# Optimization experiments

Hardware: AMD Instinct MI355X
Metric: run time of the kernel (lower is better)

Reference implementation:

```python
import jax, jax.numpy as jnp
import numpy as np

H, D = 8, 16
HD = H * D
SCALE0 = float(1.0 / np.sqrt(D * 1))   # degree-0 dot-product scale (order m=1)
SCALE1 = float(1.0 / np.sqrt(D * 3))   # degree-1 dot-product scale (order m=3)
SHARED = float(np.sqrt(0.5))           # shared_scale = sqrt(1/2) for DOT_PROD + SHARED
NEG = -1e9


def _split_heads_q(x):  # (b,n,HD,m) -> (b,H,n,D,m)
    b, n, _, m = x.shape
    return x.reshape(b, n, H, D, m).transpose(0, 2, 1, 3, 4)


def _split_heads_k(x):  # (b,n,N,HD,m) -> (b,H,n,N,D,m)
    b, n, N, _, m = x.shape
    return x.reshape(b, n, N, H, D, m).transpose(0, 3, 1, 2, 4, 5)


def _augment_kv(k, v, feats, W_self, null_k, null_v):
    # attend_self: VNLinear self key/value; use_null_kv: learned null tokens.
    b, n = feats.shape[:2]
    m = feats.shape[-1]
    skv = jnp.einsum('oc,bncm->bnom', W_self, feats)          # (b,n,2HD,m)
    sk, sv = jnp.split(skv, 2, axis=-2)
    sk = _split_heads_q(sk)[:, :, :, None]                     # (b,H,n,1,D,m)
    sv = _split_heads_q(sv)[:, :, :, None]
    nk = jnp.broadcast_to(null_k[None, :, None, None], (b, H, n, 1, D, m))
    nv = jnp.broadcast_to(null_v[None, :, None, None], (b, H, n, 1, D, m))
    k = jnp.concatenate([nk, sk, k], axis=3)                   # (b,H,n,2+N,D,m)
    v = jnp.concatenate([nv, sv, v], axis=3)
    return k, v


def _merge_heads(x):  # (b,H,n,D,m) -> (b,n,HD,m)
    b, _, n, _, m = x.shape
    return x.transpose(0, 2, 1, 3, 4).reshape(b, n, HD, m)


def _forward(q0, k0, v0, q1, k1, v1, feats0, feats1, edges,
             W_self_kv0, W_self_kv1, W_bias, self_bias, null_bias,
             null_k0, null_v0, null_k1, null_v1, head_weights1,
             W_out0, W_out1, neighbor_mask):
    b, n, N = edges.shape[:3]
    q0h, k0h, v0h = _split_heads_q(q0), _split_heads_k(k0), _split_heads_k(v0)
    q1h, k1h, v1h = _split_heads_q(q1), _split_heads_k(k1), _split_heads_k(v1)
    k0h, v0h = _augment_kv(k0h, v0h, feats0, W_self_kv0, null_k0, null_v0)
    k1h, v1h = _augment_kv(k1h, v1h, feats1, W_self_kv1, null_k1, null_v1)

    # pair bias for degree 0 (to_order==1); prepend null/self bias columns
    edge_bias = jnp.einsum('bnje,he->bhnj', edges, W_bias)     # (b,H,n,N)
    nb = jnp.broadcast_to(null_bias[None, :, None, None], (b, H, n, 1))
    sb = jnp.broadcast_to(self_bias[None, :, None, None], (b, H, n, 1))
    bias = jnp.concatenate([nb, sb, edge_bias], axis=-1)        # (b,H,n,2+N)

    sim0 = jnp.einsum('bhndm,bhnjdm->bhnj', q0h, k0h) * SCALE0 + bias
    w1 = jax.nn.softplus(head_weights1)                         # (1,H,1,1)
    sim1 = jnp.einsum('bhndm,bhnjdm->bhnj', q1h, k1h) * (SCALE1 * w1)

    total = (sim0 + sim1) * SHARED
    mask = jnp.concatenate(
        [jnp.ones((b, 1, n, 2), dtype=bool),                    # null + self always valid
         neighbor_mask[:, None]], axis=-1)
    total = jnp.where(mask, total, NEG)
    attn = jax.nn.softmax(total, axis=-1)                       # shared across degrees

    out0 = _merge_heads(jnp.einsum('bhnj,bhnjdm->bhndm', attn, v0h))
    out1 = _merge_heads(jnp.einsum('bhnj,bhnjdm->bhndm', attn, v1h))

    y0 = jnp.einsum('oc,bncm->bnom', W_out0, out0)              # FiberLinear deg 0
    y1 = jnp.einsum('oc,bncm->bnom', W_out1, out1)              # FiberLinear deg 1
    return y0, y1


def setup_inputs() -> dict:
    key = jax.random.key(0)
    ks = jax.random.split(key, 20)
    b, n, N, e = 1, 2048, 32, 32
    d0, d1 = 128, 64
    f = lambda k, s: jax.random.normal(k, s, dtype=jnp.float32) * 0.1
    return {
        'q0': f(ks[0], (b, n, HD, 1)), 'k0': f(ks[1], (b, n, N, HD, 1)), 'v0': f(ks[2], (b, n, N, HD, 1)),
        'q1': f(ks[3], (b, n, HD, 3)), 'k1': f(ks[4], (b, n, N, HD, 3)), 'v1': f(ks[5], (b, n, N, HD, 3)),
        'feats0': f(ks[6], (b, n, d0, 1)), 'feats1': f(ks[7], (b, n, d1, 3)),
        'edges': f(ks[8], (b, n, N, e)),
        'W_self_kv0': f(ks[9], (2 * HD, d0)), 'W_self_kv1': f(ks[10], (2 * HD, d1)),
        'W_bias': f(ks[11], (H, e)),
        'self_bias': jnp.zeros((H,), jnp.float32), 'null_bias': jnp.zeros((H,), jnp.float32),
        'null_k0': jnp.zeros((H, D, 1), jnp.float32), 'null_v0': jnp.zeros((H, D, 1), jnp.float32),
        'null_k1': jnp.zeros((H, D, 3), jnp.float32), 'null_v1': jnp.zeros((H, D, 3), jnp.float32),
        'head_weights1': jnp.full((1, H, 1, 1), float(np.log(np.e - 1.0)), jnp.float32),
        'W_out0': f(ks[12], (d0, HD)), 'W_out1': f(ks[13], (d1, HD)),
        'neighbor_mask': jax.random.uniform(ks[14], (b, n, N)) > 0.1,
    }


def reference(q0, k0, v0, q1, k1, v1, feats0, feats1, edges,
              W_self_kv0, W_self_kv1, W_bias, self_bias, null_bias,
              null_k0, null_v0, null_k1, null_v1, head_weights1,
              W_out0, W_out1, neighbor_mask):
    return _forward(q0, k0, v0, q1, k1, v1, feats0, feats1, edges,
                    W_self_kv0, W_self_kv1, W_bias, self_bias, null_bias,
                    null_k0, null_v0, null_k1, null_v1, head_weights1,
                    W_out0, W_out1, neighbor_mask)
```

## Files before the change

### kernel.cpp

```cpp
#include <hip/hip_runtime.h>
#include <hip/hip_bf16.h>

constexpr int kH  = 8;
constexpr int kD  = 16;
constexpr int kHD = 128;
constexpr int kN  = 32;
constexpr int kE  = 32;
constexpr int kD0 = 128;
constexpr int kD1 = 64;

constexpr float SCALE0   = 0.25f;
constexpr float SCALE1   = 0.14433756729740643f;
constexpr float SHARED_S = 0.70710678118654752f;
constexpr float NEGV     = -1e9f;

__global__ __launch_bounds__(256) void se3_attn_kernel(
    const float* __restrict__ q0, const float* __restrict__ k0, const float* __restrict__ v0,
    const float* __restrict__ q1, const float* __restrict__ k1, const float* __restrict__ v1,
    const float* __restrict__ feats0, const float* __restrict__ feats1,
    const float* __restrict__ edges,
    const float* __restrict__ Wskv0, const float* __restrict__ Wskv1,
    const float* __restrict__ Wbias, const float* __restrict__ self_bias,
    const float* __restrict__ null_bias,
    const float* __restrict__ nk0, const float* __restrict__ nv0,
    const float* __restrict__ nk1, const float* __restrict__ nv1,
    const float* __restrict__ hw1,
    const float* __restrict__ Wout0, const float* __restrict__ Wout1,
    const int* __restrict__ nmask,
    float* __restrict__ out, int n_total)
{
  const int i = blockIdx.x;
  const int t = threadIdx.x;

  __shared__ float q0s[kH * 17];
  __shared__ float q1s[kH * 49];
  __shared__ float f0s[kD0];
  __shared__ float f1s[kD1 * 3];
  __shared__ float edg[kN * 33];
  __shared__ float wbT[kE * kH];
  __shared__ float w1s[kH];
  __shared__ float sk0[kHD], sv0[kHD];
  __shared__ float sk1[kHD * 3], sv1[kHD * 3];
  __shared__ float sc[kH][34];
  __shared__ float o0[kHD];
  __shared__ float o1[kHD * 3];

  {
    if (t < kHD) {
      int h = t >> 4, d = t & 15;
      q0s[h * 17 + d] = q0[(size_t)i * kHD + t];
    }
    for (int u = t; u < kHD * 3; u += 256) {
      int c = u / 3, m = u - c * 3;
      int h = c >> 4, d = c & 15;
      q1s[h * 49 + d * 3 + m] = q1[(size_t)i * kHD * 3 + u];
    }
    if (t < kD0) f0s[t] = feats0[(size_t)i * kD0 + t];
    if (t < kD1 * 3) f1s[t] = feats1[(size_t)i * kD1 * 3 + t];
    for (int u = t; u < kN * kE; u += 256) {
      int j = u >> 5, e = u & 31;
      edg[j * 33 + e] = edges[(size_t)i * kN * kE + u];
    }
    if (t < kH * kE) {
      int h = t >> 5, e = t & 31;
      wbT[e * 8 + h] = Wbias[t];
    }
    if (t < kH) {
      float x = hw1[t];
      w1s[t] = log1pf(expf(x));
    }
  }
  __syncthreads();

  {
    const int o = t;
    float acc = 0.f;
    const float4* wrow = (const float4*)(Wskv0 + o * kD0);
    #pragma unroll
    for (int g = 0; g < 32; ++g) {
      float4 w = wrow[g];
      int cb = g * 4;
      acc += w.x * f0s[cb + 0] + w.y * f0s[cb + 1] + w.z * f0s[cb + 2] + w.w * f0s[cb + 3];
    }
    if (o < kHD) sk0[o] = acc; else sv0[o - kHD] = acc;
    float a0 = 0.f, a1 = 0.f, a2 = 0.f;
    const float4* wrow1 = (const float4*)(Wskv1 + o * kD1);
    #pragma unroll
    for (int g = 0; g < 16; ++g) {
      float4 w = wrow1[g];
      float wv[4] = {w.x, w.y, w.z, w.w};
      int cb = g * 4;
      #pragma unroll
      for (int q = 0; q < 4; ++q) {
        int c3 = (cb + q) * 3;
        a0 += wv[q] * f1s[c3 + 0];
        a1 += wv[q] * f1s[c3 + 1];
        a2 += wv[q] * f1s[c3 + 2];
      }
    }
    if (o < kHD) { sk1[o*3+0] = a0; sk1[o*3+1] = a1; sk1[o*3+2] = a2; }
    else { int p = (o - kHD) * 3; sv1[p+0] = a0; sv1[p+1] = a1; sv1[p+2] = a2; }
  }

  {
    const int j = t >> 3, h = t & 7;
    float bias = 0.f;
    #pragma unroll
    for (int e = 0; e < kE; ++e) bias += edg[j * 33 + e] * wbT[e * 8 + h];
    float s0 = 0.f;
    {
      const float4* kr = (const float4*)(k0 + (size_t)(i * kN + j) * kHD + h * kD);
      #pragma unroll
      for (int g = 0; g < 4; ++g) {
        float4 w = kr[g];
        int x = h * 17 + g * 4;
        s0 += w.x * q0s[x + 0] + w.y * q0s[x + 1] + w.z * q0s[x + 2] + w.w * q0s[x + 3];
      }
    }
    float s1 = 0.f;
    {
      const float4* kr1 = (const float4*)(k1 + (size_t)(i * kN + j) * kHD * 3 + h * 48);
      #pragma unroll
      for (int g = 0; g < 12; ++g) {
        float4 w = kr1[g];
        int x = h * 49 + g * 4;
        s1 += w.x * q1s[x + 0] + w.y * q1s[x + 1] + w.z * q1s[x + 2] + w.w * q1s[x + 3];
      }
    }
    float total = (s0 * SCALE0 + bias + s1 * SCALE1 * w1s[h]) * SHARED_S;
    bool valid = nmask[(size_t)i * kN + j] != 0;
    sc[h][2 + j] = valid ? total : NEGV;
  }
  __syncthreads();

  if (t < 2 * kH) {
    int h = t & 7;
    bool is_self = t >= kH;
    float s0 = 0.f, s1 = 0.f, bias;
    if (is_self) {
      #pragma unroll
      for (int d = 0; d < kD; ++d) s0 += q0s[h * 17 + d] * sk0[h * kD + d];
      #pragma unroll
      for (int x = 0; x < 48; ++x) s1 += q1s[h * 49 + x] * sk1[h * 48 + x];
      bias = self_bias[h];
    } else {
      #pragma unroll
      for (int d = 0; d < kD; ++d) s0 += q0s[h * 17 + d] * nk0[h * kD + d];
      #pragma unroll
      for (int x = 0; x < 48; ++x) s1 += q1s[h * 49 + x] * nk1[h * 48 + x];
      bias = null_bias[h];
    }
    float total = (s0 * SCALE0 + bias + s1 * SCALE1 * w1s[h]) * SHARED_S;
    sc[h][is_self ? 1 : 0] = total;
  }
  __syncthreads();

  if (t < kH) {
    float mx = -1e30f;
    #pragma unroll
    for (int j = 0; j < 34; ++j) mx = fmaxf(mx, sc[t][j]);
    float sum = 0.f;
    #pragma unroll
    for (int j = 0; j < 34; ++j) sum += __expf(sc[t][j] - mx);
    float inv = 1.f / sum;
    #pragma unroll
    for (int j = 0; j < 34; ++j) sc[t][j] = __expf(sc[t][j] - mx) * inv;
  }
  __syncthreads();

  if (t < 64) {
    const int c0 = 2 * t;
    const int h = t >> 3;
    float ax = sc[h][0] * nv0[c0]     + sc[h][1] * sv0[c0];
    float ay = sc[h][0] * nv0[c0 + 1] + sc[h][1] * sv0[c0 + 1];
    const float2* vp = (const float2*)(v0 + (size_t)i * kN * kHD) + t;
    #pragma unroll
    for (int j = 0; j < kN; ++j) {
      float2 p = vp[j * 64];
      float a = sc[h][2 + j];
      ax += a * p.x; ay += a * p.y;
    }
    o0[c0] = ax; o0[c0 + 1] = ay;
  } else {
    const int u = t - 64;
    const int f0i = 2 * u;
    const int h = u / 24;
    float ax = sc[h][0] * nv1[f0i]     + sc[h][1] * sv1[f0i];
    float ay = sc[h][0] * nv1[f0i + 1] + sc[h][1] * sv1[f0i + 1];
    const float2* vp = (const float2*)(v1 + (size_t)i * kN * kHD * 3) + u;
    #pragma unroll
    for (int j = 0; j < kN; ++j) {
      float2 p = vp[j * 192];
      float a = sc[h][2 + j];
      ax += a * p.x; ay += a * p.y;
    }
    o1[f0i] = ax; o1[f0i + 1] = ay;
  }
  __syncthreads();

  for (int u = t; u < 320; u += 256) {
    if (u < 128) {
      const int o = u;
      float acc = 0.f;
      const float4* wr = (const float4*)(Wout0 + o * kHD);
      #pragma unroll
      for (int g = 0; g < 32; ++g) {
        float4 w = wr[g];
        int cb = g * 4;
        acc += w.x * o0[cb + 0] + w.y * o0[cb + 1] + w.z * o0[cb + 2] + w.w * o0[cb + 3];
      }
      out[(size_t)i * kHD + o] = acc;
    } else {
      const int v2 = u - 128;
      const int o = v2 / 3, m = v2 - o * 3;
      float acc = 0.f;
      const float4* wr = (const float4*)(Wout1 + o * kHD);
      #pragma unroll
      for (int g = 0; g < 32; ++g) {
        float4 w = wr[g];
        int cb = g * 4;
        acc += w.x * o1[(cb + 0) * 3 + m] + w.y * o1[(cb + 1) * 3 + m]
             + w.z * o1[(cb + 2) * 3 + m] + w.w * o1[(cb + 3) * 3 + m];
      }
      out[(size_t)n_total * kHD + (size_t)i * 192 + v2] = acc;
    }
  }
}

extern "C" void kernel_launch(void* const* d_in, const int* in_sizes, int n_in,
                              void* d_out, int out_size, void* d_ws, size_t ws_size,
                              hipStream_t stream) {
  const int n = in_sizes[0] / kHD;
  se3_attn_kernel<<<n, 256, 0, stream>>>(
      (const float*)d_in[0],  (const float*)d_in[1],  (const float*)d_in[2],
      (const float*)d_in[3],  (const float*)d_in[4],  (const float*)d_in[5],
      (const float*)d_in[6],  (const float*)d_in[7],  (const float*)d_in[8],
      (const float*)d_in[9],  (const float*)d_in[10], (const float*)d_in[11],
      (const float*)d_in[12], (const float*)d_in[13], (const float*)d_in[14],
      (const float*)d_in[15], (const float*)d_in[16], (const float*)d_in[17],
      (const float*)d_in[18], (const float*)d_in[19], (const float*)d_in[20],
      (const int*)d_in[21],
      (float*)d_out, n);
}
```

Baseline: 379.2 us.

## Split fused attention kernel into three kernels staged through workspace

Splits the single per-node kernel into three launches: self key/value projection with null/self scores, neighbor similarity plus softmax, and value aggregation plus output projection. Intermediates (scores, self values) go through global workspace instead of shared memory. This may lower per-kernel register and shared-memory pressure and raise occupancy, at the cost of extra launches, global round trips, and reloading q in two kernels.

Result: slower. 389.6 us (+2.7%).

```diff
diff --git a/kernel.cpp b/kernel.cpp
--- a/kernel.cpp
+++ b/kernel.cpp
@@ -14,170 +14,197 @@
 constexpr float SHARED_S = 0.70710678118654752f;
 constexpr float NEGV     = -1e9f;
 
-__global__ __launch_bounds__(256) void se3_attn_kernel(
-    const float* __restrict__ q0, const float* __restrict__ k0, const float* __restrict__ v0,
-    const float* __restrict__ q1, const float* __restrict__ k1, const float* __restrict__ v1,
+
+__global__ __launch_bounds__(256) void k1_selfkv(
+    const float* __restrict__ q0, const float* __restrict__ q1,
     const float* __restrict__ feats0, const float* __restrict__ feats1,
-    const float* __restrict__ edges,
     const float* __restrict__ Wskv0, const float* __restrict__ Wskv1,
-    const float* __restrict__ Wbias, const float* __restrict__ self_bias,
-    const float* __restrict__ null_bias,
-    const float* __restrict__ nk0, const float* __restrict__ nv0,
-    const float* __restrict__ nk1, const float* __restrict__ nv1,
+    const float* __restrict__ self_bias, const float* __restrict__ null_bias,
+    const float* __restrict__ nk0, const float* __restrict__ nk1,
     const float* __restrict__ hw1,
+    float* __restrict__ ws_sc, float* __restrict__ ws_sv0, float* __restrict__ ws_sv1)
+{
+  const int i = blockIdx.x;
+  const int t = threadIdx.x;
+  __shared__ float f0s[kD0];
+  __shared__ float f1s[kD1 * 3];
+  __shared__ float q0s[kHD];
+  __shared__ float q1s[kHD * 3];
+  __shared__ float sk0[kHD];
+  __shared__ float sk1[kHD * 3];
+  __shared__ float w1s[kH];
+
+  if (t < kD0)     f0s[t] = feats0[(size_t)i * kD0 + t];
+  if (t < kD1 * 3) f1s[t] = feats1[(size_t)i * kD1 * 3 + t];
+  if (t < kHD)     q0s[t] = q0[(size_t)i * kHD + t];
+  for (int u = t; u < kHD * 3; u += 256) q1s[u] = q1[(size_t)i * kHD * 3 + u];
+  if (t < kH) w1s[t] = log1pf(expf(hw1[t]));
+  __syncthreads();
+
+  float acc = 0.f;
+  {
+    const float4* wr = (const float4*)(Wskv0 + t * kD0);
+    #pragma unroll
+    for (int g = 0; g < 32; ++g) {
+      float4 w = wr[g];
+      int c = g * 4;
+      acc += w.x * f0s[c] + w.y * f0s[c + 1] + w.z * f0s[c + 2] + w.w * f0s[c + 3];
+    }
+  }
+  float a0 = 0.f, a1 = 0.f, a2 = 0.f;
+  {
+    const float4* wr = (const float4*)(Wskv1 + t * kD1);
+    #pragma unroll
+    for (int g = 0; g < 16; ++g) {
+      float4 w = wr[g];
+      int c = g * 4;
+      a0 += w.x * f1s[(c + 0) * 3 + 0] + w.y * f1s[(c + 1) * 3 + 0]
+          + w.z * f1s[(c + 2) * 3 + 0] + w.w * f1s[(c + 3) * 3 + 0];
+      a1 += w.x * f1s[(c + 0) * 3 + 1] + w.y * f1s[(c + 1) * 3 + 1]
+          + w.z * f1s[(c + 2) * 3 + 1] + w.w * f1s[(c + 3) * 3 + 1];
+      a2 += w.x * f1s[(c + 0) * 3 + 2] + w.y * f1s[(c + 1) * 3 + 2]
+          + w.z * f1s[(c + 2) * 3 + 2] + w.w * f1s[(c + 3) * 3 + 2];
+    }
+  }
+  if (t < kHD) {
+    sk0[t] = acc;
+    sk1[t * 3 + 0] = a0; sk1[t * 3 + 1] = a1; sk1[t * 3 + 2] = a2;
+  } else {
+    const int o = t - kHD;
+    ws_sv0[(size_t)i * kHD + o] = acc;
+    float* sp = ws_sv1 + (size_t)i * kHD * 3 + o * 3;
+    sp[0] = a0; sp[1] = a1; sp[2] = a2;
+  }
+  __syncthreads();
+
+  if (t < 2 * kH) {
+    const int h = t & 7;
+    const bool is_self = t >= kH;
+    float s0 = 0.f, s1 = 0.f, bias;
+    if (is_self) {
+      #pragma unroll
+      for (int d = 0; d < kD; ++d) s0 += q0s[h * kD + d] * sk0[h * kD + d];
+      #pragma unroll
+      for (int x = 0; x < 48; ++x) s1 += q1s[h * 48 + x] * sk1[h * 48 + x];
+      bias = self_bias[h];
+    } else {
+      #pragma unroll
+      for (int d = 0; d < kD; ++d) s0 += q0s[h * kD + d] * nk0[h * kD + d];
+      #pragma unroll
+      for (int x = 0; x < 48; ++x) s1 += q1s[h * 48 + x] * nk1[h * 48 + x];
+      bias = null_bias[h];
+    }
+    float total = (s0 * SCALE0 + bias + s1 * SCALE1 * w1s[h]) * SHARED_S;
+    ws_sc[(size_t)i * 272 + h * 34 + (is_self ? 1 : 0)] = total;
+  }
+}
+
+__global__ __launch_bounds__(256) void k2_sims(
+    const float* __restrict__ q0, const float* __restrict__ q1,
+    const float* __restrict__ k0, const float* __restrict__ k1,
+    const float* __restrict__ edges, const float* __restrict__ Wbias,
+    const float* __restrict__ hw1, const int* __restrict__ nmask,
+    float* __restrict__ ws_sc)
+{
+  const int i = blockIdx.x;
+  const int t = threadIdx.x;
+  __shared__ float q0s[kH * 17];
+  __shared__ float q1s[kH * 49];
+  __shared__ float edg[kN * 33];
+  __shared__ float wbT[kE * kH];
+  __shared__ float w1s[kH];
+  __shared__ float scL[kH][34];
+
+  if (t < kHD) {
+    int h = t >> 4, d = t & 15;
+    q0s[h * 17 + d] = q0[(size_t)i * kHD + t];
+  }
+  for (int u = t; u < kHD * 3; u += 256) {
+    int c = u / 3, m = u - c * 3;
+    int h = c >> 4, d = c & 15;
+    q1s[h * 49 + d * 3 + m] = q1[(size_t)i * kHD * 3 + u];
+  }
+  for (int u = t; u < kN * kE; u += 256) {
+    int j = u >> 5, e = u & 31;
+    edg[j * 33 + e] = edges[(size_t)i * kN * kE + u];
+  }
+  if (t < kH * kE) {
+    int h = t >> 5, e = t & 31;
+    wbT[e * 8 + h] = Wbias[t];
+  }
+  if (t < kH) w1s[t] = log1pf(expf(hw1[t]));
+  if (t < 16) scL[t & 7][t >> 3] = ws_sc[(size_t)i * 272 + (t & 7) * 34 + (t >> 3)];
+  __syncthreads();
+
+  {
+    const int j = t >> 3, h = t & 7;
+    float bias = 0.f;
+    #pragma unroll
+    for (int e = 0; e < kE; ++e) bias += edg[j * 33 + e] * wbT[e * 8 + h];
+    float s0 = 0.f;
+    {
+      const float4* kr = (const float4*)(k0 + (size_t)(i * kN + j) * kHD + h * kD);
+      #pragma unroll
+      for (int g = 0; g < 4; ++g) {
+        float4 w = kr[g];
+        int x = h * 17 + g * 4;
+        s0 += w.x * q0s[x] + w.y * q0s[x + 1] + w.z * q0s[x + 2] + w.w * q0s[x + 3];
+      }
+    }
+    float s1 = 0.f;
+    {
+      const float4* kr = (const float4*)(k1 + (size_t)(i * kN + j) * kHD * 3 + h * 48);
+      #pragma unroll
+      for (int g = 0; g < 12; ++g) {
+        float4 w = kr[g];
+        int x = h * 49 + g * 4;
+        s1 += w.x * q1s[x] + w.y * q1s[x + 1] + w.z * q1s[x + 2] + w.w * q1s[x + 3];
+      }
+    }
+    float total = (s0 * SCALE0 + bias + s1 * SCALE1 * w1s[h]) * SHARED_S;
+    bool valid = nmask[(size_t)i * kN + j] != 0;
+    scL[h][2 + j] = valid ? total : NEGV;
+  }
+  __syncthreads();
+
+  if (t < kH) {
+    float mx = -1e30f;
+    #pragma unroll
+    for (int j = 0; j < 34; ++j) mx = fmaxf(mx, scL[t][j]);
+    float sum = 0.f;
+    #pragma unroll
+    for (int j = 0; j < 34; ++j) sum += __expf(scL[t][j] - mx);
+    float inv = 1.f / sum;
+    float* dst = ws_sc + (size_t)i * 272 + t * 34;
+    #pragma unroll
+    for (int j = 0; j < 34; ++j) dst[j] = __expf(scL[t][j] - mx) * inv;
+  }
+}
+
+__global__ __launch_bounds__(256) void k3_out(
+    const float* __restrict__ v0, const float* __restrict__ v1,
+    const float* __restrict__ nv0, const float* __restrict__ nv1,
+    const float* __restrict__ ws_sc,
+    const float* __restrict__ ws_sv0, const float* __restrict__ ws_sv1,
     const float* __restrict__ Wout0, const float* __restrict__ Wout1,
-    const int* __restrict__ nmask,
     float* __restrict__ out, int n_total)
 {
   const int i = blockIdx.x;
   const int t = threadIdx.x;
-
-  __shared__ float q0s[kH * 17];
-  __shared__ float q1s[kH * 49];
-  __shared__ float f0s[kD0];
-  __shared__ float f1s[kD1 * 3];
-  __shared__ float edg[kN * 33];
-  __shared__ float wbT[kE * kH];
-  __shared__ float w1s[kH];
-  __shared__ float sk0[kHD], sv0[kHD];
-  __shared__ float sk1[kHD * 3], sv1[kHD * 3];
-  __shared__ float sc[kH][34];
   __shared__ float o0[kHD];
   __shared__ float o1[kHD * 3];
-
-  {
-    if (t < kHD) {
-      int h = t >> 4, d = t & 15;
-      q0s[h * 17 + d] = q0[(size_t)i * kHD + t];
-    }
-    for (int u = t; u < kHD * 3; u += 256) {
-      int c = u / 3, m = u - c * 3;
-      int h = c >> 4, d = c & 15;
-      q1s[h * 49 + d * 3 + m] = q1[(size_t)i * kHD * 3 + u];
-    }
-    if (t < kD0) f0s[t] = feats0[(size_t)i * kD0 + t];
-    if (t < kD1 * 3) f1s[t] = feats1[(size_t)i * kD1 * 3 + t];
-    for (int u = t; u < kN * kE; u += 256) {
-      int j = u >> 5, e = u & 31;
-      edg[j * 33 + e] = edges[(size_t)i * kN * kE + u];
-    }
-    if (t < kH * kE) {
-      int h = t >> 5, e = t & 31;
-      wbT[e * 8 + h] = Wbias[t];
-    }
-    if (t < kH) {
-      float x = hw1[t];
-      w1s[t] = log1pf(expf(x));
-    }
-  }
-  __syncthreads();
-
-  {
-    const int o = t;
-    float acc = 0.f;
-    const float4* wrow = (const float4*)(Wskv0 + o * kD0);
-    #pragma unroll
-    for (int g = 0; g < 32; ++g) {
-      float4 w = wrow[g];
-      int cb = g * 4;
-      acc += w.x * f0s[cb + 0] + w.y * f0s[cb + 1] + w.z * f0s[cb + 2] + w.w * f0s[cb + 3];
-    }
-    if (o < kHD) sk0[o] = acc; else sv0[o - kHD] = acc;
-    float a0 = 0.f, a1 = 0.f, a2 = 0.f;
-    const float4* wrow1 = (const float4*)(Wskv1 + o * kD1);
-    #pragma unroll
-    for (int g = 0; g < 16; ++g) {
-      float4 w = wrow1[g];
-      float wv[4] = {w.x, w.y, w.z, w.w};
-      int cb = g * 4;
-      #pragma unroll
-      for (int q = 0; q < 4; ++q) {
-        int c3 = (cb + q) * 3;
-        a0 += wv[q] * f1s[c3 + 0];
-        a1 += wv[q] * f1s[c3 + 1];
-        a2 += wv[q] * f1s[c3 + 2];
-      }
-    }
-    if (o < kHD) { sk1[o*3+0] = a0; sk1[o*3+1] = a1; sk1[o*3+2] = a2; }
-    else { int p = (o - kHD) * 3; sv1[p+0] = a0; sv1[p+1] = a1; sv1[p+2] = a2; }
-  }
-
-  {
-    const int j = t >> 3, h = t & 7;
-    float bias = 0.f;
-    #pragma unroll
-    for (int e = 0; e < kE; ++e) bias += edg[j * 33 + e] * wbT[e * 8 + h];
-    float s0 = 0.f;
-    {
-      const float4* kr = (const float4*)(k0 + (size_t)(i * kN + j) * kHD + h * kD);
-      #pragma unroll
-      for (int g = 0; g < 4; ++g) {
-        float4 w = kr[g];
-        int x = h * 17 + g * 4;
-        s0 += w.x * q0s[x + 0] + w.y * q0s[x + 1] + w.z * q0s[x + 2] + w.w * q0s[x + 3];
-      }
-    }
-    float s1 = 0.f;
-    {
-      const float4* kr1 = (const float4*)(k1 + (size_t)(i * kN + j) * kHD * 3 + h * 48);
-      #pragma unroll
-      for (int g = 0; g < 12; ++g) {
-        float4 w = kr1[g];
-        int x = h * 49 + g * 4;
-        s1 += w.x * q1s[x + 0] + w.y * q1s[x + 1] + w.z * q1s[x + 2] + w.w * q1s[x + 3];
-      }
-    }
-    float total = (s0 * SCALE0 + bias + s1 * SCALE1 * w1s[h]) * SHARED_S;
-    bool valid = nmask[(size_t)i * kN + j] != 0;
-    sc[h][2 + j] = valid ? total : NEGV;
-  }
-  __syncthreads();
-
-  if (t < 2 * kH) {
-    int h = t & 7;
-    bool is_self = t >= kH;
-    float s0 = 0.f, s1 = 0.f, bias;
-    if (is_self) {
-      #pragma unroll
-      for (int d = 0; d < kD; ++d) s0 += q0s[h * 17 + d] * sk0[h * kD + d];
-      #pragma unroll
-      for (int x = 0; x < 48; ++x) s1 += q1s[h * 49 + x] * sk1[h * 48 + x];
-      bias = self_bias[h];
-    } else {
-      #pragma unroll
-      for (int d = 0; d < kD; ++d) s0 += q0s[h * 17 + d] * nk0[h * kD + d];
-      #pragma unroll
-      for (int x = 0; x < 48; ++x) s1 += q1s[h * 49 + x] * nk1[h * 48 + x];
-      bias = null_bias[h];
-    }
-    float total = (s0 * SCALE0 + bias + s1 * SCALE1 * w1s[h]) * SHARED_S;
-    sc[h][is_self ? 1 : 0] = total;
-  }
-  __syncthreads();
-
-  if (t < kH) {
-    float mx = -1e30f;
-    #pragma unroll
-    for (int j = 0; j < 34; ++j) mx = fmaxf(mx, sc[t][j]);
-    float sum = 0.f;
-    #pragma unroll
-    for (int j = 0; j < 34; ++j) sum += __expf(sc[t][j] - mx);
-    float inv = 1.f / sum;
-    #pragma unroll
-    for (int j = 0; j < 34; ++j) sc[t][j] = __expf(sc[t][j] - mx) * inv;
-  }
-  __syncthreads();
 
   if (t < 64) {
     const int c0 = 2 * t;
     const int h = t >> 3;
-    float ax = sc[h][0] * nv0[c0]     + sc[h][1] * sv0[c0];
-    float ay = sc[h][0] * nv0[c0 + 1] + sc[h][1] * sv0[c0 + 1];
+    const float* at = ws_sc + (size_t)i * 272 + h * 34;
+    float ax = at[0] * nv0[c0]     + at[1] * ws_sv0[(size_t)i * kHD + c0];
+    float ay = at[0] * nv0[c0 + 1] + at[1] * ws_sv0[(size_t)i * kHD + c0 + 1];
     const float2* vp = (const float2*)(v0 + (size_t)i * kN * kHD) + t;
     #pragma unroll
     for (int j = 0; j < kN; ++j) {
       float2 p = vp[j * 64];
-      float a = sc[h][2 + j];
+      float a = at[2 + j];
       ax += a * p.x; ay += a * p.y;
     }
     o0[c0] = ax; o0[c0 + 1] = ay;
@@ -185,13 +212,14 @@
     const int u = t - 64;
     const int f0i = 2 * u;
     const int h = u / 24;
-    float ax = sc[h][0] * nv1[f0i]     + sc[h][1] * sv1[f0i];
-    float ay = sc[h][0] * nv1[f0i + 1] + sc[h][1] * sv1[f0i + 1];
+    const float* at = ws_sc + (size_t)i * 272 + h * 34;
+    float ax = at[0] * nv1[f0i]     + at[1] * ws_sv1[(size_t)i * kHD * 3 + f0i];
+    float ay = at[0] * nv1[f0i + 1] + at[1] * ws_sv1[(size_t)i * kHD * 3 + f0i + 1];
     const float2* vp = (const float2*)(v1 + (size_t)i * kN * kHD * 3) + u;
     #pragma unroll
     for (int j = 0; j < kN; ++j) {
       float2 p = vp[j * 192];
-      float a = sc[h][2 + j];
+      float a = at[2 + j];
       ax += a * p.x; ay += a * p.y;
     }
     o1[f0i] = ax; o1[f0i + 1] = ay;
@@ -200,16 +228,15 @@
 
   for (int u = t; u < 320; u += 256) {
     if (u < 128) {
-      const int o = u;
       float acc = 0.f;
-      const float4* wr = (const float4*)(Wout0 + o * kHD);
+      const float4* wr = (const float4*)(Wout0 + u * kHD);
       #pragma unroll
       for (int g = 0; g < 32; ++g) {
         float4 w = wr[g];
-        int cb = g * 4;
-        acc += w.x * o0[cb + 0] + w.y * o0[cb + 1] + w.z * o0[cb + 2] + w.w * o0[cb + 3];
-      }
-      out[(size_t)i * kHD + o] = acc;
+        int c = g * 4;
+        acc += w.x * o0[c] + w.y * o0[c + 1] + w.z * o0[c + 2] + w.w * o0[c + 3];
+      }
+      out[(size_t)i * kHD + u] = acc;
     } else {
       const int v2 = u - 128;
       const int o = v2 / 3, m = v2 - o * 3;
@@ -218,9 +245,9 @@
       #pragma unroll
       for (int g = 0; g < 32; ++g) {
         float4 w = wr[g];
-        int cb = g * 4;
-        acc += w.x * o1[(cb + 0) * 3 + m] + w.y * o1[(cb + 1) * 3 + m]
-             + w.z * o1[(cb + 2) * 3 + m] + w.w * o1[(cb + 3) * 3 + m];
+        int c = g * 4;
+        acc += w.x * o1[(c + 0) * 3 + m] + w.y * o1[(c + 1) * 3 + m]
+             + w.z * o1[(c + 2) * 3 + m] + w.w * o1[(c + 3) * 3 + m];
       }
       out[(size_t)n_total * kHD + (size_t)i * 192 + v2] = acc;
     }
@@ -231,14 +258,38 @@
                               void* d_out, int out_size, void* d_ws, size_t ws_size,
                               hipStream_t stream) {
   const int n = in_sizes[0] / kHD;
-  se3_attn_kernel<<<n, 256, 0, stream>>>(
-      (const float*)d_in[0],  (const float*)d_in[1],  (const float*)d_in[2],
-      (const float*)d_in[3],  (const float*)d_in[4],  (const float*)d_in[5],
-      (const float*)d_in[6],  (const float*)d_in[7],  (const float*)d_in[8],
-      (const float*)d_in[9],  (const float*)d_in[10], (const float*)d_in[11],
-      (const float*)d_in[12], (const float*)d_in[13], (const float*)d_in[14],
-      (const float*)d_in[15], (const float*)d_in[16], (const float*)d_in[17],
-      (const float*)d_in[18], (const float*)d_in[19], (const float*)d_in[20],
-      (const int*)d_in[21],
-      (float*)d_out, n);
-}
+  const float* q0     = (const float*)d_in[0];
+  const float* k0     = (const float*)d_in[1];
+  const float* v0     = (const float*)d_in[2];
+  const float* q1     = (const float*)d_in[3];
+  const float* k1     = (const float*)d_in[4];
+  const float* v1     = (const float*)d_in[5];
+  const float* feats0 = (const float*)d_in[6];
+  const float* feats1 = (const float*)d_in[7];
+  const float* edges  = (const float*)d_in[8];
+  const float* Wskv0  = (const float*)d_in[9];
+  const float* Wskv1  = (const float*)d_in[10];
+  const float* Wbias  = (const float*)d_in[11];
+  const float* sbias  = (const float*)d_in[12];
+  const float* nbias  = (const float*)d_in[13];
+  const float* nk0    = (const float*)d_in[14];
+  const float* nv0    = (const float*)d_in[15];
+  const float* nk1    = (const float*)d_in[16];
+  const float* nv1    = (const float*)d_in[17];
+  const float* hw1    = (const float*)d_in[18];
+  const float* Wout0  = (const float*)d_in[19];
+  const float* Wout1  = (const float*)d_in[20];
+  const int*   nmask  = (const int*)d_in[21];
+
+  float* ws     = (float*)d_ws;
+  float* ws_sc  = ws;
+  float* ws_sv0 = ws + (size_t)n * 272;
+  float* ws_sv1 = ws + (size_t)n * 272 + (size_t)n * 128;
+
+  k1_selfkv<<<n, 256, 0, stream>>>(q0, q1, feats0, feats1, Wskv0, Wskv1,
+                                   sbias, nbias, nk0, nk1, hw1,
+                                   ws_sc, ws_sv0, ws_sv1);
+  k2_sims<<<n, 256, 0, stream>>>(q0, q1, k0, k1, edges, Wbias, hw1, nmask, ws_sc);
+  k3_out<<<n, 256, 0, stream>>>(v0, v1, nv0, nv1, ws_sc, ws_sv0, ws_sv1,
+                                Wout0, Wout1, (float*)d_out, n);
+}
```
